# Kernel tuning notes

Hardware: AMD Instinct MI355X
Metric: run time of the kernel (lower is better)

The kernel has to match this reference:

```python
import jax, jax.numpy as jnp
import numpy as np

N, E, D, C, L = 50000, 800000, 128, 10, 3
TAU = 0.5
EPS = 1e-5


def _ln(h, g, b):
    m = jnp.mean(h, axis=-1, keepdims=True)
    v = jnp.mean((h - m) ** 2, axis=-1, keepdims=True)
    return (h - m) * jax.lax.rsqrt(v + EPS) * g + b


def _gumbel_hard(logits, gnoise, tau):
    # gumbel_softmax(hard=True): straight-through one-hot of softmax((logits+g)/tau)
    y_soft = jax.nn.softmax((logits + gnoise) / tau, axis=-1)
    idx = jnp.argmax(y_soft, axis=-1)
    y_hard = jax.nn.one_hot(idx, logits.shape[-1], dtype=y_soft.dtype)
    return jax.lax.stop_gradient(y_hard - y_soft) + y_soft


def setup_inputs() -> dict:
    key = jax.random.key(0)
    ks = jax.random.split(key, 20)
    s = lambda *sh: 1.0 / np.sqrt(sh[0])
    inp = {
        "x": jax.random.normal(ks[0], (N, D), jnp.float32),
        "edge_index": jax.random.randint(ks[1], (2, E), 0, N, jnp.int64),
        # encoder (node_encoder Linear in_dim->env_dim)
        "W_enc": jax.random.normal(ks[2], (D, D), jnp.float32) * s(D),
        "b_enc": jnp.zeros((D,), jnp.float32),
        # shared hidden LayerNorm
        "ln_g": jnp.ones((D,), jnp.float32),
        "ln_b": jnp.zeros((D,), jnp.float32),
        # env GNN layers (root / neighbor weights + bias), L layers
        "Wr": jax.random.normal(ks[3], (L, D, D), jnp.float32) * s(D),
        "Wn": jax.random.normal(ks[4], (L, D, D), jnp.float32) * s(D),
        "bl": jnp.zeros((L, D), jnp.float32),
        # in/out action nets (1 layer each, env_dim -> 2 logits)
        "Wa_in_r": jax.random.normal(ks[5], (D, 2), jnp.float32) * s(D),
        "Wa_in_n": jax.random.normal(ks[6], (D, 2), jnp.float32) * s(D),
        "ba_in": jnp.zeros((2,), jnp.float32),
        "Wa_out_r": jax.random.normal(ks[7], (D, 2), jnp.float32) * s(D),
        "Wa_out_n": jax.random.normal(ks[8], (D, 2), jnp.float32) * s(D),
        "ba_out": jnp.zeros((2,), jnp.float32),
        # decoder (dec_num_layers=1 -> single Linear env_dim -> num_classes)
        "W_dec": jax.random.normal(ks[9], (D, C), jnp.float32) * s(D),
        "b_dec": jnp.zeros((C,), jnp.float32),
        # pre-sampled Gumbel noise per layer for in/out action gates
        "gin": jax.random.gumbel(ks[10], (L, N, 2), jnp.float32),
        "gout": jax.random.gumbel(ks[11], (L, N, 2), jnp.float32),
    }
    return inp


def reference(x, edge_index, W_enc, b_enc, ln_g, ln_b, Wr, Wn, bl,
              Wa_in_r, Wa_in_n, ba_in, Wa_out_r, Wa_out_n, ba_out,
              W_dec, b_dec, gin, gout):
    u, v = edge_index[0], edge_index[1]
    n = x.shape[0]
    # node encoder + (use_encoders=False) dropout(0)+act
    h = jax.nn.relu(x @ W_enc + b_enc)
    node_states = []
    for l in range(L):
        hn = _ln(h, ln_g, ln_b)
        # unweighted neighbor aggregation shared by both action nets
        agg = jax.ops.segment_sum(hn[u], v, num_segments=n)  # [N, D]
        in_logits = hn @ Wa_in_r + agg @ Wa_in_n + ba_in
        out_logits = hn @ Wa_out_r + agg @ Wa_out_n + ba_out
        in_p = _gumbel_hard(in_logits, gin[l], TAU)
        out_p = _gumbel_hard(out_logits, gout[l], TAU)
        # edge gate: listen prob of target * broadcast prob of source
        ew = in_p[v, 0] * out_p[u, 0]  # [E]
        aggw = jax.ops.segment_sum(ew[:, None] * hn[u], v, num_segments=n)
        out = jax.nn.relu(hn @ Wr[l] + aggw @ Wn[l] + bl[l])
        # node state bookkeeping: 0 standard, 1 broadcast-only, 2 listen-only, 3 isolated
        act = jax.lax.stop_gradient(ew)
        is_b = (jax.ops.segment_max(act, u, num_segments=n) > 0.5).astype(jnp.int32)
        is_l = (jax.ops.segment_max(act, v, num_segments=n) > 0.5).astype(jnp.int32)
        node_states.append(3 - 2 * is_b - is_l)
        h = hn + out  # skip connection (onto the normalized x, as in the source)
    h = _ln(h, ln_g, ln_b)
    result = h @ W_dec + b_dec
    return result, jnp.stack(node_states)
```

## Files before the change

kernel.cpp:

```cpp
#include <hip/hip_runtime.h>

#define DIM 128
#define NCLS 10

__global__ void k_hist(const int* __restrict__ ei, int E, int* __restrict__ deg) {
    int e = blockIdx.x * 256 + threadIdx.x;
    if (e < E) atomicAdd(&deg[ei[E + e]], 1);
}

__global__ void k_scan1(const int* __restrict__ deg, int* __restrict__ row_start,
                        int* __restrict__ bsum, int n) {
    int tid = threadIdx.x;
    int base = blockIdx.x * 1024 + tid * 4;
    int v0 = 0, v1 = 0, v2 = 0, v3 = 0;
    if (base + 3 < n) {
        int4 t = *(const int4*)(deg + base);
        v0 = t.x; v1 = t.y; v2 = t.z; v3 = t.w;
    } else {
        if (base + 0 < n) v0 = deg[base + 0];
        if (base + 1 < n) v1 = deg[base + 1];
        if (base + 2 < n) v2 = deg[base + 2];
        if (base + 3 < n) v3 = deg[base + 3];
    }
    int s = v0 + v1 + v2 + v3;
    int lane = tid & 63, w = tid >> 6;
    int inc = s;
#pragma unroll
    for (int o = 1; o < 64; o <<= 1) {
        int t = __shfl_up(inc, o);
        if (lane >= o) inc += t;
    }
    __shared__ int wsum[4];
    if (lane == 63) wsum[w] = inc;
    __syncthreads();
    int woff = 0;
    for (int i = 0; i < w; i++) woff += wsum[i];
    int run = woff + inc - s;
    if (base + 0 < n) row_start[base + 0] = run; run += v0;
    if (base + 1 < n) row_start[base + 1] = run; run += v1;
    if (base + 2 < n) row_start[base + 2] = run; run += v2;
    if (base + 3 < n) row_start[base + 3] = run;
    if (tid == 0) bsum[blockIdx.x] = wsum[0] + wsum[1] + wsum[2] + wsum[3];
}

__global__ void k_scan2(int* __restrict__ bsum, int nb) {
    int tid = threadIdx.x;
    if (nb <= 64) {
        int v = (tid < nb) ? bsum[tid] : 0;
        int inc = v;
#pragma unroll
        for (int o = 1; o < 64; o <<= 1) {
            int t = __shfl_up(inc, o);
            if (tid >= o) inc += t;
        }
        if (tid < nb) bsum[tid] = inc - v;
    } else if (tid == 0) {
        int acc = 0;
        for (int i = 0; i < nb; i++) { int t = bsum[i]; bsum[i] = acc; acc += t; }
    }
}

__global__ void k_scan3(int* __restrict__ row_start, int* __restrict__ cursor,
                        const int* __restrict__ bsum, int n, int E) {
    int i = blockIdx.x * 256 + threadIdx.x;
    if (i < n) {
        int r = row_start[i] + bsum[i >> 10];
        row_start[i] = r;
        cursor[i] = r;
    }
    if (i == n) row_start[n] = E;
}

__global__ void k_fill(const int* __restrict__ ei, int E, int* __restrict__ cursor,
                       int* __restrict__ csr) {
    int e = blockIdx.x * 256 + threadIdx.x;
    if (e < E) {
        int u = ei[e], v = ei[E + e];
        int pos = atomicAdd(&cursor[v], 1);
        csr[pos] = u;
    }
}

__global__ void k_action(const float* __restrict__ proj, const int* __restrict__ row_start,
                         const int* __restrict__ csr,
                         const float* __restrict__ bain, const float* __restrict__ baon,
                         const float* __restrict__ gin_l, const float* __restrict__ gout_l,
                         int* __restrict__ in_bit, int* __restrict__ out_bit,
                         int* __restrict__ is_b, int n) {
    int v = blockIdx.x * 256 + threadIdx.x;
    if (v >= n) return;
    is_b[v] = 0;
    int b0 = row_start[v], b1 = row_start[v + 1];
    double a0 = 0.0, a1 = 0.0, a2 = 0.0, a3 = 0.0;
    for (int e = b0; e < b1; e++) {
        int u = csr[e];
        float4 p = *(const float4*)(proj + (size_t)u * 8);
        a0 += p.x; a1 += p.y; a2 += p.z; a3 += p.w;
    }
    float4 r = *(const float4*)(proj + (size_t)v * 8 + 4);
    float2 gi = *(const float2*)(gin_l + (size_t)v * 2);
    float2 go = *(const float2*)(gout_l + (size_t)v * 2);
    float li0 = (float)a0 + r.x + bain[0] + gi.x;
    float li1 = (float)a1 + r.y + bain[1] + gi.y;
    float lo0 = (float)a2 + r.z + baon[0] + go.x;
    float lo1 = (float)a3 + r.w + baon[1] + go.y;
    in_bit[v]  = (li0 >= li1) ? 1 : 0;
    out_bit[v] = (lo0 >= lo1) ? 1 : 0;
}

__global__ void k_aggw(const float* __restrict__ hn, const int* __restrict__ row_start,
                       const int* __restrict__ csr, const int* __restrict__ in_bit,
                       const int* __restrict__ out_bit,
                       int* __restrict__ is_b, int* __restrict__ is_l,
                       float* __restrict__ aggw, int n) {
    int wid = (blockIdx.x * 256 + threadIdx.x) >> 6;
    int lane = threadIdx.x & 63;
    if (wid >= n) return;
    int d0 = lane * 2;
    double ax = 0.0, ay = 0.0;
    int anyg = 0;
    if (in_bit[wid]) {
        int base = row_start[wid], end = row_start[wid + 1];
        for (int off = base; off < end; off += 64) {
            int m = min(64, end - off);
            int myu = 0, myb = 0;
            if (lane < m) { myu = csr[off + lane]; myb = out_bit[myu]; }
            unsigned long long mask = __ballot(myb != 0);
            anyg |= (mask != 0ull);
            while (mask) {
                int i = __ffsll((unsigned long long)mask) - 1;
                mask &= mask - 1;
                int u = __shfl(myu, i);
                if (lane == 0) is_b[u] = 1;
                float2 t = *(const float2*)(hn + (size_t)u * DIM + d0);
                ax += t.x; ay += t.y;
            }
        }
    }
    if (lane == 0) is_l[wid] = anyg;
    ((float2*)(aggw + (size_t)wid * DIM))[lane] = make_float2((float)ax, (float)ay);
}

template <int HAS_B, int SKIP, int DO_LN, int DO_PROJ, int DO_STATES, int DO_DEC, int WRITE_H>
__launch_bounds__(256)
__attribute__((amdgpu_waves_per_eu(4, 4)))
__global__ void k_gemm(const float* __restrict__ A, const float* __restrict__ W1,
                       const float* __restrict__ B, const float* __restrict__ W2,
                       const float* __restrict__ bias,
                       const float* __restrict__ ln_g, const float* __restrict__ ln_b,
                       const float* __restrict__ Wain, const float* __restrict__ Waon,
                       const float* __restrict__ Wair, const float* __restrict__ Waor,
                       const int* __restrict__ is_b, const int* __restrict__ is_l,
                       const float* __restrict__ Wdec, const float* __restrict__ bdec,
                       float* __restrict__ out, float* __restrict__ proj,
                       float* __restrict__ states_l, float* __restrict__ dec_out, int n) {
    __shared__ float sW[32][128];
    __shared__ float sA[64][36];
    int tid = threadIdx.x;
    int rowBase = blockIdx.x * 64;
    int ty = tid >> 4, tx = tid & 15;
    int c0 = tx * 4, c1 = 64 + tx * 4;
    float acc[4][8];
#pragma unroll
    for (int i = 0; i < 4; i++)
#pragma unroll
        for (int j = 0; j < 8; j++) acc[i][j] = 0.f;

    for (int p = 0; p < 1 + HAS_B; p++) {
        const float* Ap = p ? B : A;
        const float* Wp = p ? W2 : W1;
        for (int kc = 0; kc < DIM; kc += 32) {
            __syncthreads();
            {
                const float4* src = (const float4*)(Wp + kc * DIM);
                float4* dst = (float4*)(&sW[0][0]);
#pragma unroll
                for (int i = 0; i < 4; i++) {
                    int j = i * 256 + tid;
                    dst[j] = src[j];
                }
#pragma unroll
                for (int i = 0; i < 2; i++) {
                    int j = i * 256 + tid;
                    int r = j >> 3, c4 = (j & 7) * 4;
                    float4 va = (rowBase + r < n)
                        ? *(const float4*)(Ap + (size_t)(rowBase + r) * DIM + kc + c4)
                        : make_float4(0.f, 0.f, 0.f, 0.f);
                    *(float4*)&sA[r][c4] = va;
                }
            }
            __syncthreads();
#pragma unroll
            for (int kk = 0; kk < 32; kk += 4) {
                float4 a[4];
#pragma unroll
                for (int i = 0; i < 4; i++) a[i] = *(const float4*)&sA[i * 16 + ty][kk];
#pragma unroll
                for (int q = 0; q < 4; q++) {
                    float4 w0 = *(const float4*)&sW[kk + q][c0];
                    float4 w1 = *(const float4*)&sW[kk + q][c1];
#pragma unroll
                    for (int i = 0; i < 4; i++) {
                        float av = (&a[i].x)[q];
                        acc[i][0] += av * w0.x;
                        acc[i][1] += av * w0.y;
                        acc[i][2] += av * w0.z;
                        acc[i][3] += av * w0.w;
                        acc[i][4] += av * w1.x;
                        acc[i][5] += av * w1.y;
                        acc[i][6] += av * w1.z;
                        acc[i][7] += av * w1.w;
                    }
                }
            }
        }
    }

    float* sWd = (float*)&sW[0][0];
    if (DO_DEC) {
        __syncthreads();
        for (int i = tid; i < NCLS * DIM; i += 256) {
            int d = i / NCLS, c = i % NCLS;
            sWd[c * DIM + d] = Wdec[i];
        }
        __syncthreads();
    }

    float4 bias0 = *(const float4*)&bias[c0];
    float4 bias1 = *(const float4*)&bias[c1];
    float bv[8] = {bias0.x, bias0.y, bias0.z, bias0.w, bias1.x, bias1.y, bias1.z, bias1.w};
    float gv[8], bbv[8];
    if (DO_LN) {
        float4 g0 = *(const float4*)&ln_g[c0];
        float4 g1 = *(const float4*)&ln_g[c1];
        float4 lb0 = *(const float4*)&ln_b[c0];
        float4 lb1 = *(const float4*)&ln_b[c1];
        gv[0]=g0.x; gv[1]=g0.y; gv[2]=g0.z; gv[3]=g0.w; gv[4]=g1.x; gv[5]=g1.y; gv[6]=g1.z; gv[7]=g1.w;
        bbv[0]=lb0.x; bbv[1]=lb0.y; bbv[2]=lb0.z; bbv[3]=lb0.w; bbv[4]=lb1.x; bbv[5]=lb1.y; bbv[6]=lb1.z; bbv[7]=lb1.w;
    }

#pragma unroll
    for (int i = 0; i < 4; i++) {
        int r = rowBase + i * 16 + ty;
        if (r >= n) continue;
        float v[8];
        if (SKIP) {
            float4 s0 = *(const float4*)(A + (size_t)r * DIM + c0);
            float4 s1 = *(const float4*)(A + (size_t)r * DIM + c1);
            float sv[8] = {s0.x, s0.y, s0.z, s0.w, s1.x, s1.y, s1.z, s1.w};
#pragma unroll
            for (int j = 0; j < 8; j++) v[j] = fmaxf(acc[i][j] + bv[j], 0.f) + sv[j];
        } else {
#pragma unroll
            for (int j = 0; j < 8; j++) v[j] = fmaxf(acc[i][j] + bv[j], 0.f);
        }
        if (DO_LN) {
            float s = 0.f, q = 0.f;
#pragma unroll
            for (int j = 0; j < 8; j++) { s += v[j]; q += v[j] * v[j]; }
#pragma unroll
            for (int o = 1; o < 16; o <<= 1) { s += __shfl_xor(s, o); q += __shfl_xor(q, o); }
            float m = s * (1.f / DIM);
            float var = q * (1.f / DIM) - m * m;
            float inv = rsqrtf(var + 1e-5f);
#pragma unroll
            for (int j = 0; j < 8; j++) v[j] = (v[j] - m) * inv * gv[j] + bbv[j];
        }
        if (WRITE_H) {
            *(float4*)(out + (size_t)r * DIM + c0) = make_float4(v[0], v[1], v[2], v[3]);
            *(float4*)(out + (size_t)r * DIM + c1) = make_float4(v[4], v[5], v[6], v[7]);
        }
        if (DO_STATES) {
            if (tx == 0) states_l[r] = (float)(3 - 2 * is_b[r] - is_l[r]);
        }
        if (DO_PROJ) {
            float pv[8];
            auto dotw = [&](const float* Wm, float& p0, float& p1) {
                float4 q0 = *(const float4*)(Wm + c0 * 2);
                float4 q1 = *(const float4*)(Wm + c0 * 2 + 4);
                float4 q2 = *(const float4*)(Wm + c1 * 2);
                float4 q3 = *(const float4*)(Wm + c1 * 2 + 4);
                p0 = v[0]*q0.x + v[1]*q0.z + v[2]*q1.x + v[3]*q1.z
                   + v[4]*q2.x + v[5]*q2.z + v[6]*q3.x + v[7]*q3.z;
                p1 = v[0]*q0.y + v[1]*q0.w + v[2]*q1.y + v[3]*q1.w
                   + v[4]*q2.y + v[5]*q2.w + v[6]*q3.y + v[7]*q3.w;
            };
            dotw(Wain, pv[0], pv[1]);
            dotw(Waon, pv[2], pv[3]);
            dotw(Wair, pv[4], pv[5]);
            dotw(Waor, pv[6], pv[7]);
#pragma unroll
            for (int o = 1; o < 16; o <<= 1)
#pragma unroll
                for (int j = 0; j < 8; j++) pv[j] += __shfl_xor(pv[j], o);
            if (tx == 0) {
                *(float4*)(proj + (size_t)r * 8)     = make_float4(pv[0], pv[1], pv[2], pv[3]);
                *(float4*)(proj + (size_t)r * 8 + 4) = make_float4(pv[4], pv[5], pv[6], pv[7]);
            }
        }
        if (DO_DEC) {
            float p[NCLS];
#pragma unroll
            for (int c = 0; c < NCLS; c++) {
                float4 wd0 = *(const float4*)&sWd[c * DIM + c0];
                float4 wd1 = *(const float4*)&sWd[c * DIM + c1];
                p[c] = v[0]*wd0.x + v[1]*wd0.y + v[2]*wd0.z + v[3]*wd0.w
                     + v[4]*wd1.x + v[5]*wd1.y + v[6]*wd1.z + v[7]*wd1.w;
            }
#pragma unroll
            for (int o = 1; o < 16; o <<= 1)
#pragma unroll
                for (int c = 0; c < NCLS; c++) p[c] += __shfl_xor(p[c], o);
            if (tx == 0) {
#pragma unroll
                for (int c = 0; c < NCLS; c++) dec_out[(size_t)r * NCLS + c] = p[c] + bdec[c];
            }
        }
    }
}

extern "C" void kernel_launch(void* const* d_in, const int* in_sizes, int n_in,
                              void* d_out, int out_size, void* d_ws, size_t ws_size,
                              hipStream_t stream) {
    const float* x      = (const float*)d_in[0];
    const int*   ei     = (const int*)d_in[1];
    const float* W_enc  = (const float*)d_in[2];
    const float* b_enc  = (const float*)d_in[3];
    const float* ln_g   = (const float*)d_in[4];
    const float* ln_b   = (const float*)d_in[5];
    const float* Wr     = (const float*)d_in[6];
    const float* Wn     = (const float*)d_in[7];
    const float* bl     = (const float*)d_in[8];
    const float* Wair   = (const float*)d_in[9];
    const float* Wain   = (const float*)d_in[10];
    const float* bain   = (const float*)d_in[11];
    const float* Waor   = (const float*)d_in[12];
    const float* Waon   = (const float*)d_in[13];
    const float* baon   = (const float*)d_in[14];
    const float* W_dec  = (const float*)d_in[15];
    const float* b_dec  = (const float*)d_in[16];
    const float* gin    = (const float*)d_in[17];
    const float* gout   = (const float*)d_in[18];

    int n = in_sizes[0] / DIM;
    int E = in_sizes[1] / 2;
    const int L = 3;

    char* wsp = (char*)d_ws;
    auto alloc = [&](size_t bytes) { char* p = wsp; wsp += (bytes + 255) / 256 * 256; return p; };
    float* hn   = (float*)alloc((size_t)n * DIM * 4);
    float* aggw = (float*)alloc((size_t)n * DIM * 4);
    float* proj = (float*)alloc((size_t)n * 8 * 4);
    int* deg       = (int*)alloc((size_t)n * 4);
    int* row_start = (int*)alloc((size_t)(n + 1) * 4);
    int* cursor    = (int*)alloc((size_t)n * 4);
    int* csr       = (int*)alloc((size_t)E * 4);
    int* in_bit    = (int*)alloc((size_t)n * 4);
    int* out_bit   = (int*)alloc((size_t)n * 4);
    int* bsum      = (int*)alloc((size_t)256 * 4);
    int* is_b      = (int*)alloc((size_t)n * 4);
    int* is_l      = (int*)alloc((size_t)n * 4);

    float* out_res    = (float*)d_out;
    float* out_states = out_res + (size_t)n * NCLS;

    int ebl = (E + 255) / 256;
    int nbl = (n + 255) / 256;
    int wbl = (n + 3) / 4;
    int gbl = (n + 63) / 64;
    int nb  = (n + 1023) / 1024;

    hipMemsetAsync(deg, 0, (size_t)n * 4, stream);
    k_hist<<<ebl, 256, 0, stream>>>(ei, E, deg);
    k_scan1<<<nb, 256, 0, stream>>>(deg, row_start, bsum, n);
    k_scan2<<<1, 64, 0, stream>>>(bsum, nb);
    k_scan3<<<(n + 256) / 256, 256, 0, stream>>>(row_start, cursor, bsum, n, E);
    k_fill<<<ebl, 256, 0, stream>>>(ei, E, cursor, csr);

    k_gemm<0, 0, 1, 1, 0, 0, 1><<<gbl, 256, 0, stream>>>(
        x, W_enc, nullptr, nullptr, b_enc, ln_g, ln_b,
        Wain, Waon, Wair, Waor, nullptr, nullptr, nullptr, nullptr,
        hn, proj, nullptr, nullptr, n);

    for (int l = 0; l < L; l++) {
        k_action<<<nbl, 256, 0, stream>>>(proj, row_start, csr, bain, baon,
                                          gin + (size_t)l * n * 2, gout + (size_t)l * n * 2,
                                          in_bit, out_bit, is_b, n);
        k_aggw<<<wbl, 256, 0, stream>>>(hn, row_start, csr, in_bit, out_bit,
                                        is_b, is_l, aggw, n);
        if (l + 1 < L) {
            k_gemm<1, 1, 1, 1, 1, 0, 1><<<gbl, 256, 0, stream>>>(
                hn, Wr + (size_t)l * DIM * DIM, aggw, Wn + (size_t)l * DIM * DIM,
                bl + (size_t)l * DIM, ln_g, ln_b,
                Wain, Waon, Wair, Waor, is_b, is_l, nullptr, nullptr,
                hn, proj, out_states + (size_t)l * n, nullptr, n);
        } else {
            k_gemm<1, 1, 1, 0, 1, 1, 0><<<gbl, 256, 0, stream>>>(
                hn, Wr + (size_t)l * DIM * DIM, aggw, Wn + (size_t)l * DIM * DIM,
                bl + (size_t)l * DIM, ln_g, ln_b,
                Wain, Waon, Wair, Waor, is_b, is_l, W_dec, b_dec,
                hn, nullptr, out_states + (size_t)l * n, out_res, n);
        }
    }
}
```

Measured before the change: 485.3 us.

## Project node features before aggregation to run GEMMs ahead of gated gather

Uses linearity to compute hn·Wr and hn·Wn in one two-column-block GEMM before the gated neighbour sum. A new post kernel then gathers the projected rows, adds bias, ReLU, the skip connection and LayerNorm, and computes the action projections or decoder logits. This removes the dependence of the GEMM on the aggregated tensor and fuses the epilogue into the gather pass. In exchange it writes and reads two N×D intermediates per layer instead of one, and the gather now sums projected values in a different order. State output is moved into k_action plus a final small kernel.

```diff
diff --git a/kernel.cpp b/kernel.cpp
--- a/kernel.cpp
+++ b/kernel.cpp
@@ -86,9 +86,11 @@
                          const float* __restrict__ bain, const float* __restrict__ baon,
                          const float* __restrict__ gin_l, const float* __restrict__ gout_l,
                          int* __restrict__ in_bit, int* __restrict__ out_bit,
-                         int* __restrict__ is_b, int n) {
+                         int* __restrict__ is_b, const int* __restrict__ is_l,
+                         float* __restrict__ states_prev, int n) {
     int v = blockIdx.x * 256 + threadIdx.x;
     if (v >= n) return;
+    if (states_prev) states_prev[v] = (float)(3 - 2 * is_b[v] - is_l[v]);
     is_b[v] = 0;
     int b0 = row_start[v], b1 = row_start[v + 1];
     double a0 = 0.0, a1 = 0.0, a2 = 0.0, a3 = 0.0;
@@ -108,15 +110,170 @@
     out_bit[v] = (lo0 >= lo1) ? 1 : 0;
 }
 
-__global__ void k_aggw(const float* __restrict__ hn, const int* __restrict__ row_start,
-                       const int* __restrict__ csr, const int* __restrict__ in_bit,
-                       const int* __restrict__ out_bit,
+template <int ENC>
+__launch_bounds__(256)
+__attribute__((amdgpu_waves_per_eu(4, 4)))
+__global__ void k_gemm(const float* __restrict__ A,
+                       const float* __restrict__ W1, const float* __restrict__ W2,
+                       const float* __restrict__ bias,
+                       const float* __restrict__ ln_g, const float* __restrict__ ln_b,
+                       const float* __restrict__ Wain, const float* __restrict__ Waon,
+                       const float* __restrict__ Wair, const float* __restrict__ Waor,
+                       float* __restrict__ out1, float* __restrict__ out2,
+                       float* __restrict__ proj, int n) {
+    __shared__ float sW[32][128];
+    __shared__ float sA[64][36];
+    int tid = threadIdx.x;
+    int rowBase = blockIdx.y * 64;
+    const float* Wp = (ENC || blockIdx.x == 0) ? W1 : W2;
+    float* outp = (ENC || blockIdx.x == 0) ? out1 : out2;
+    int ty = tid >> 4, tx = tid & 15;
+    int c0 = tx * 4, c1 = 64 + tx * 4;
+    float acc[4][8];
+#pragma unroll
+    for (int i = 0; i < 4; i++)
+#pragma unroll
+        for (int j = 0; j < 8; j++) acc[i][j] = 0.f;
+
+    for (int kc = 0; kc < DIM; kc += 32) {
+        __syncthreads();
+        {
+            const float4* src = (const float4*)(Wp + kc * DIM);
+            float4* dst = (float4*)(&sW[0][0]);
+#pragma unroll
+            for (int i = 0; i < 4; i++) {
+                int j = i * 256 + tid;
+                dst[j] = src[j];
+            }
+#pragma unroll
+            for (int i = 0; i < 2; i++) {
+                int j = i * 256 + tid;
+                int r = j >> 3, c4 = (j & 7) * 4;
+                float4 va = (rowBase + r < n)
+                    ? *(const float4*)(A + (size_t)(rowBase + r) * DIM + kc + c4)
+                    : make_float4(0.f, 0.f, 0.f, 0.f);
+                *(float4*)&sA[r][c4] = va;
+            }
+        }
+        __syncthreads();
+#pragma unroll
+        for (int kk = 0; kk < 32; kk += 4) {
+            float4 a[4];
+#pragma unroll
+            for (int i = 0; i < 4; i++) a[i] = *(const float4*)&sA[i * 16 + ty][kk];
+#pragma unroll
+            for (int q = 0; q < 4; q++) {
+                float4 w0 = *(const float4*)&sW[kk + q][c0];
+                float4 w1 = *(const float4*)&sW[kk + q][c1];
+#pragma unroll
+                for (int i = 0; i < 4; i++) {
+                    float av = (&a[i].x)[q];
+                    acc[i][0] += av * w0.x;
+                    acc[i][1] += av * w0.y;
+                    acc[i][2] += av * w0.z;
+                    acc[i][3] += av * w0.w;
+                    acc[i][4] += av * w1.x;
+                    acc[i][5] += av * w1.y;
+                    acc[i][6] += av * w1.z;
+                    acc[i][7] += av * w1.w;
+                }
+            }
+        }
+    }
+
+    if (!ENC) {
+#pragma unroll
+        for (int i = 0; i < 4; i++) {
+            int r = rowBase + i * 16 + ty;
+            if (r >= n) continue;
+            *(float4*)(outp + (size_t)r * DIM + c0) = make_float4(acc[i][0], acc[i][1], acc[i][2], acc[i][3]);
+            *(float4*)(outp + (size_t)r * DIM + c1) = make_float4(acc[i][4], acc[i][5], acc[i][6], acc[i][7]);
+        }
+        return;
+    }
+
+    float4 bias0 = *(const float4*)&bias[c0];
+    float4 bias1 = *(const float4*)&bias[c1];
+    float bv[8] = {bias0.x, bias0.y, bias0.z, bias0.w, bias1.x, bias1.y, bias1.z, bias1.w};
+    float4 g0 = *(const float4*)&ln_g[c0];
+    float4 g1 = *(const float4*)&ln_g[c1];
+    float4 lb0 = *(const float4*)&ln_b[c0];
+    float4 lb1 = *(const float4*)&ln_b[c1];
+    float gv[8]  = {g0.x, g0.y, g0.z, g0.w, g1.x, g1.y, g1.z, g1.w};
+    float bbv[8] = {lb0.x, lb0.y, lb0.z, lb0.w, lb1.x, lb1.y, lb1.z, lb1.w};
+
+#pragma unroll
+    for (int i = 0; i < 4; i++) {
+        int r = rowBase + i * 16 + ty;
+        if (r >= n) continue;
+        float v[8];
+#pragma unroll
+        for (int j = 0; j < 8; j++) v[j] = fmaxf(acc[i][j] + bv[j], 0.f);
+        float s = 0.f, q = 0.f;
+#pragma unroll
+        for (int j = 0; j < 8; j++) { s += v[j]; q += v[j] * v[j]; }
+#pragma unroll
+        for (int o = 1; o < 16; o <<= 1) { s += __shfl_xor(s, o); q += __shfl_xor(q, o); }
+        float m = s * (1.f / DIM);
+        float var = q * (1.f / DIM) - m * m;
+        float inv = rsqrtf(var + 1e-5f);
+#pragma unroll
+        for (int j = 0; j < 8; j++) v[j] = (v[j] - m) * inv * gv[j] + bbv[j];
+        *(float4*)(out1 + (size_t)r * DIM + c0) = make_float4(v[0], v[1], v[2], v[3]);
+        *(float4*)(out1 + (size_t)r * DIM + c1) = make_float4(v[4], v[5], v[6], v[7]);
+
+        float pv[8];
+        auto dotw = [&](const float* Wm, float& p0, float& p1) {
+            float4 q0 = *(const float4*)(Wm + c0 * 2);
+            float4 q1 = *(const float4*)(Wm + c0 * 2 + 4);
+            float4 q2 = *(const float4*)(Wm + c1 * 2);
+            float4 q3 = *(const float4*)(Wm + c1 * 2 + 4);
+            p0 = v[0]*q0.x + v[1]*q0.z + v[2]*q1.x + v[3]*q1.z
+               + v[4]*q2.x + v[5]*q2.z + v[6]*q3.x + v[7]*q3.z;
+            p1 = v[0]*q0.y + v[1]*q0.w + v[2]*q1.y + v[3]*q1.w
+               + v[4]*q2.y + v[5]*q2.w + v[6]*q3.y + v[7]*q3.w;
+        };
+        dotw(Wain, pv[0], pv[1]);
+        dotw(Waon, pv[2], pv[3]);
+        dotw(Wair, pv[4], pv[5]);
+        dotw(Waor, pv[6], pv[7]);
+#pragma unroll
+        for (int o = 1; o < 16; o <<= 1)
+#pragma unroll
+            for (int j = 0; j < 8; j++) pv[j] += __shfl_xor(pv[j], o);
+        if (tx == 0) {
+            *(float4*)(proj + (size_t)r * 8)     = make_float4(pv[0], pv[1], pv[2], pv[3]);
+            *(float4*)(proj + (size_t)r * 8 + 4) = make_float4(pv[4], pv[5], pv[6], pv[7]);
+        }
+    }
+}
+
+template <int DO_PROJ, int DO_DEC>
+__global__ void k_post(const float* __restrict__ y, const float* __restrict__ z,
+                       float* __restrict__ hn,
+                       const int* __restrict__ row_start, const int* __restrict__ csr,
+                       const int* __restrict__ in_bit, const int* __restrict__ out_bit,
                        int* __restrict__ is_b, int* __restrict__ is_l,
-                       float* __restrict__ aggw, int n) {
-    int wid = (blockIdx.x * 256 + threadIdx.x) >> 6;
-    int lane = threadIdx.x & 63;
+                       const float* __restrict__ bl_l,
+                       const float* __restrict__ ln_g, const float* __restrict__ ln_b,
+                       const float* __restrict__ Wain, const float* __restrict__ Waon,
+                       const float* __restrict__ Wair, const float* __restrict__ Waor,
+                       const float* __restrict__ Wdec, const float* __restrict__ bdec,
+                       float* __restrict__ proj, float* __restrict__ dec_out, int n) {
+    __shared__ float sWd[NCLS * DIM];
+    int tid = threadIdx.x;
+    if (DO_DEC) {
+        for (int i = tid; i < NCLS * DIM; i += 256) {
+            int d = i / NCLS, c = i % NCLS;
+            sWd[c * DIM + d] = Wdec[i];
+        }
+        __syncthreads();
+    }
+    int wid = (blockIdx.x * 256 + tid) >> 6;
+    int lane = tid & 63;
     if (wid >= n) return;
     int d0 = lane * 2;
+
     double ax = 0.0, ay = 0.0;
     int anyg = 0;
     if (in_bit[wid]) {
@@ -132,191 +289,74 @@
                 mask &= mask - 1;
                 int u = __shfl(myu, i);
                 if (lane == 0) is_b[u] = 1;
-                float2 t = *(const float2*)(hn + (size_t)u * DIM + d0);
+                float2 t = *(const float2*)(z + (size_t)u * DIM + d0);
                 ax += t.x; ay += t.y;
             }
         }
     }
     if (lane == 0) is_l[wid] = anyg;
-    ((float2*)(aggw + (size_t)wid * DIM))[lane] = make_float2((float)ax, (float)ay);
-}
-
-template <int HAS_B, int SKIP, int DO_LN, int DO_PROJ, int DO_STATES, int DO_DEC, int WRITE_H>
-__launch_bounds__(256)
-__attribute__((amdgpu_waves_per_eu(4, 4)))
-__global__ void k_gemm(const float* __restrict__ A, const float* __restrict__ W1,
-                       const float* __restrict__ B, const float* __restrict__ W2,
-                       const float* __restrict__ bias,
-                       const float* __restrict__ ln_g, const float* __restrict__ ln_b,
-                       const float* __restrict__ Wain, const float* __restrict__ Waon,
-                       const float* __restrict__ Wair, const float* __restrict__ Waor,
-                       const int* __restrict__ is_b, const int* __restrict__ is_l,
-                       const float* __restrict__ Wdec, const float* __restrict__ bdec,
-                       float* __restrict__ out, float* __restrict__ proj,
-                       float* __restrict__ states_l, float* __restrict__ dec_out, int n) {
-    __shared__ float sW[32][128];
-    __shared__ float sA[64][36];
-    int tid = threadIdx.x;
-    int rowBase = blockIdx.x * 64;
-    int ty = tid >> 4, tx = tid & 15;
-    int c0 = tx * 4, c1 = 64 + tx * 4;
-    float acc[4][8];
-#pragma unroll
-    for (int i = 0; i < 4; i++)
-#pragma unroll
-        for (int j = 0; j < 8; j++) acc[i][j] = 0.f;
-
-    for (int p = 0; p < 1 + HAS_B; p++) {
-        const float* Ap = p ? B : A;
-        const float* Wp = p ? W2 : W1;
-        for (int kc = 0; kc < DIM; kc += 32) {
-            __syncthreads();
-            {
-                const float4* src = (const float4*)(Wp + kc * DIM);
-                float4* dst = (float4*)(&sW[0][0]);
-#pragma unroll
-                for (int i = 0; i < 4; i++) {
-                    int j = i * 256 + tid;
-                    dst[j] = src[j];
-                }
-#pragma unroll
-                for (int i = 0; i < 2; i++) {
-                    int j = i * 256 + tid;
-                    int r = j >> 3, c4 = (j & 7) * 4;
-                    float4 va = (rowBase + r < n)
-                        ? *(const float4*)(Ap + (size_t)(rowBase + r) * DIM + kc + c4)
-                        : make_float4(0.f, 0.f, 0.f, 0.f);
-                    *(float4*)&sA[r][c4] = va;
-                }
-            }
-            __syncthreads();
-#pragma unroll
-            for (int kk = 0; kk < 32; kk += 4) {
-                float4 a[4];
-#pragma unroll
-                for (int i = 0; i < 4; i++) a[i] = *(const float4*)&sA[i * 16 + ty][kk];
-#pragma unroll
-                for (int q = 0; q < 4; q++) {
-                    float4 w0 = *(const float4*)&sW[kk + q][c0];
-                    float4 w1 = *(const float4*)&sW[kk + q][c1];
-#pragma unroll
-                    for (int i = 0; i < 4; i++) {
-                        float av = (&a[i].x)[q];
-                        acc[i][0] += av * w0.x;
-                        acc[i][1] += av * w0.y;
-                        acc[i][2] += av * w0.z;
-                        acc[i][3] += av * w0.w;
-                        acc[i][4] += av * w1.x;
-                        acc[i][5] += av * w1.y;
-                        acc[i][6] += av * w1.z;
-                        acc[i][7] += av * w1.w;
-                    }
-                }
-            }
-        }
-    }
-
-    float* sWd = (float*)&sW[0][0];
+
+    float2 yv = *(const float2*)(y + (size_t)wid * DIM + d0);
+    float2 h2 = *(const float2*)(hn + (size_t)wid * DIM + d0);
+    float2 b2 = *(const float2*)(bl_l + d0);
+    float vx = h2.x + fmaxf(yv.x + (float)ax + b2.x, 0.f);
+    float vy = h2.y + fmaxf(yv.y + (float)ay + b2.y, 0.f);
+
+    float s = vx + vy, q = vx * vx + vy * vy;
+#pragma unroll
+    for (int o = 32; o; o >>= 1) { s += __shfl_xor(s, o); q += __shfl_xor(q, o); }
+    float m = s * (1.f / DIM);
+    float var = q * (1.f / DIM) - m * m;
+    float inv = rsqrtf(var + 1e-5f);
+    float2 g2 = *(const float2*)(ln_g + d0);
+    float2 lb2 = *(const float2*)(ln_b + d0);
+    float ox = (vx - m) * inv * g2.x + lb2.x;
+    float oy = (vy - m) * inv * g2.y + lb2.y;
+
+    if (!DO_DEC)
+        *(float2*)(hn + (size_t)wid * DIM + d0) = make_float2(ox, oy);
+
+    if (DO_PROJ) {
+        float4 win = *(const float4*)(Wain + d0 * 2);
+        float4 won = *(const float4*)(Waon + d0 * 2);
+        float4 wir = *(const float4*)(Wair + d0 * 2);
+        float4 wor = *(const float4*)(Waor + d0 * 2);
+        float p[8];
+        p[0] = ox * win.x + oy * win.z;  p[1] = ox * win.y + oy * win.w;
+        p[2] = ox * won.x + oy * won.z;  p[3] = ox * won.y + oy * won.w;
+        p[4] = ox * wir.x + oy * wir.z;  p[5] = ox * wir.y + oy * wir.w;
+        p[6] = ox * wor.x + oy * wor.z;  p[7] = ox * wor.y + oy * wor.w;
+#pragma unroll
+        for (int o = 32; o; o >>= 1)
+#pragma unroll
+            for (int j = 0; j < 8; j++) p[j] += __shfl_xor(p[j], o);
+        if (lane == 0) {
+            *(float4*)(proj + (size_t)wid * 8)     = make_float4(p[0], p[1], p[2], p[3]);
+            *(float4*)(proj + (size_t)wid * 8 + 4) = make_float4(p[4], p[5], p[6], p[7]);
+        }
+    }
     if (DO_DEC) {
-        __syncthreads();
-        for (int i = tid; i < NCLS * DIM; i += 256) {
-            int d = i / NCLS, c = i % NCLS;
-            sWd[c * DIM + d] = Wdec[i];
-        }
-        __syncthreads();
-    }
-
-    float4 bias0 = *(const float4*)&bias[c0];
-    float4 bias1 = *(const float4*)&bias[c1];
-    float bv[8] = {bias0.x, bias0.y, bias0.z, bias0.w, bias1.x, bias1.y, bias1.z, bias1.w};
-    float gv[8], bbv[8];
-    if (DO_LN) {
-        float4 g0 = *(const float4*)&ln_g[c0];
-        float4 g1 = *(const float4*)&ln_g[c1];
-        float4 lb0 = *(const float4*)&ln_b[c0];
-        float4 lb1 = *(const float4*)&ln_b[c1];
-        gv[0]=g0.x; gv[1]=g0.y; gv[2]=g0.z; gv[3]=g0.w; gv[4]=g1.x; gv[5]=g1.y; gv[6]=g1.z; gv[7]=g1.w;
-        bbv[0]=lb0.x; bbv[1]=lb0.y; bbv[2]=lb0.z; bbv[3]=lb0.w; bbv[4]=lb1.x; bbv[5]=lb1.y; bbv[6]=lb1.z; bbv[7]=lb1.w;
-    }
-
-#pragma unroll
-    for (int i = 0; i < 4; i++) {
-        int r = rowBase + i * 16 + ty;
-        if (r >= n) continue;
-        float v[8];
-        if (SKIP) {
-            float4 s0 = *(const float4*)(A + (size_t)r * DIM + c0);
-            float4 s1 = *(const float4*)(A + (size_t)r * DIM + c1);
-            float sv[8] = {s0.x, s0.y, s0.z, s0.w, s1.x, s1.y, s1.z, s1.w};
-#pragma unroll
-            for (int j = 0; j < 8; j++) v[j] = fmaxf(acc[i][j] + bv[j], 0.f) + sv[j];
-        } else {
-#pragma unroll
-            for (int j = 0; j < 8; j++) v[j] = fmaxf(acc[i][j] + bv[j], 0.f);
-        }
-        if (DO_LN) {
-            float s = 0.f, q = 0.f;
-#pragma unroll
-            for (int j = 0; j < 8; j++) { s += v[j]; q += v[j] * v[j]; }
-#pragma unroll
-            for (int o = 1; o < 16; o <<= 1) { s += __shfl_xor(s, o); q += __shfl_xor(q, o); }
-            float m = s * (1.f / DIM);
-            float var = q * (1.f / DIM) - m * m;
-            float inv = rsqrtf(var + 1e-5f);
-#pragma unroll
-            for (int j = 0; j < 8; j++) v[j] = (v[j] - m) * inv * gv[j] + bbv[j];
-        }
-        if (WRITE_H) {
-            *(float4*)(out + (size_t)r * DIM + c0) = make_float4(v[0], v[1], v[2], v[3]);
-            *(float4*)(out + (size_t)r * DIM + c1) = make_float4(v[4], v[5], v[6], v[7]);
-        }
-        if (DO_STATES) {
-            if (tx == 0) states_l[r] = (float)(3 - 2 * is_b[r] - is_l[r]);
-        }
-        if (DO_PROJ) {
-            float pv[8];
-            auto dotw = [&](const float* Wm, float& p0, float& p1) {
-                float4 q0 = *(const float4*)(Wm + c0 * 2);
-                float4 q1 = *(const float4*)(Wm + c0 * 2 + 4);
-                float4 q2 = *(const float4*)(Wm + c1 * 2);
-                float4 q3 = *(const float4*)(Wm + c1 * 2 + 4);
-                p0 = v[0]*q0.x + v[1]*q0.z + v[2]*q1.x + v[3]*q1.z
-                   + v[4]*q2.x + v[5]*q2.z + v[6]*q3.x + v[7]*q3.z;
-                p1 = v[0]*q0.y + v[1]*q0.w + v[2]*q1.y + v[3]*q1.w
-                   + v[4]*q2.y + v[5]*q2.w + v[6]*q3.y + v[7]*q3.w;
-            };
-            dotw(Wain, pv[0], pv[1]);
-            dotw(Waon, pv[2], pv[3]);
-            dotw(Wair, pv[4], pv[5]);
-            dotw(Waor, pv[6], pv[7]);
-#pragma unroll
-            for (int o = 1; o < 16; o <<= 1)
-#pragma unroll
-                for (int j = 0; j < 8; j++) pv[j] += __shfl_xor(pv[j], o);
-            if (tx == 0) {
-                *(float4*)(proj + (size_t)r * 8)     = make_float4(pv[0], pv[1], pv[2], pv[3]);
-                *(float4*)(proj + (size_t)r * 8 + 4) = make_float4(pv[4], pv[5], pv[6], pv[7]);
-            }
-        }
-        if (DO_DEC) {
-            float p[NCLS];
-#pragma unroll
-            for (int c = 0; c < NCLS; c++) {
-                float4 wd0 = *(const float4*)&sWd[c * DIM + c0];
-                float4 wd1 = *(const float4*)&sWd[c * DIM + c1];
-                p[c] = v[0]*wd0.x + v[1]*wd0.y + v[2]*wd0.z + v[3]*wd0.w
-                     + v[4]*wd1.x + v[5]*wd1.y + v[6]*wd1.z + v[7]*wd1.w;
-            }
-#pragma unroll
-            for (int o = 1; o < 16; o <<= 1)
-#pragma unroll
-                for (int c = 0; c < NCLS; c++) p[c] += __shfl_xor(p[c], o);
-            if (tx == 0) {
-#pragma unroll
-                for (int c = 0; c < NCLS; c++) dec_out[(size_t)r * NCLS + c] = p[c] + bdec[c];
-            }
-        }
-    }
+        float p[NCLS];
+#pragma unroll
+        for (int c = 0; c < NCLS; c++) {
+            float2 w = *(const float2*)(&sWd[c * DIM + d0]);
+            p[c] = ox * w.x + oy * w.y;
+        }
+#pragma unroll
+        for (int o = 32; o; o >>= 1)
+#pragma unroll
+            for (int c = 0; c < NCLS; c++) p[c] += __shfl_xor(p[c], o);
+        if (lane == 0) {
+#pragma unroll
+            for (int c = 0; c < NCLS; c++) dec_out[(size_t)wid * NCLS + c] = p[c] + bdec[c];
+        }
+    }
+}
+
+__global__ void k_states(const int* __restrict__ is_b, const int* __restrict__ is_l,
+                         float* __restrict__ st, int n) {
+    int i = blockIdx.x * 256 + threadIdx.x;
+    if (i < n) st[i] = (float)(3 - 2 * is_b[i] - is_l[i]);
 }
 
 extern "C" void kernel_launch(void* const* d_in, const int* in_sizes, int n_in,
@@ -349,7 +389,8 @@
     char* wsp = (char*)d_ws;
     auto alloc = [&](size_t bytes) { char* p = wsp; wsp += (bytes + 255) / 256 * 256; return p; };
     float* hn   = (float*)alloc((size_t)n * DIM * 4);
-    float* aggw = (float*)alloc((size_t)n * DIM * 4);
+    float* yb   = (float*)alloc((size_t)n * DIM * 4);
+    float* zb   = (float*)alloc((size_t)n * DIM * 4);
     float* proj = (float*)alloc((size_t)n * 8 * 4);
     int* deg       = (int*)alloc((size_t)n * 4);
     int* row_start = (int*)alloc((size_t)(n + 1) * 4);
@@ -377,29 +418,33 @@
     k_scan3<<<(n + 256) / 256, 256, 0, stream>>>(row_start, cursor, bsum, n, E);
     k_fill<<<ebl, 256, 0, stream>>>(ei, E, cursor, csr);
 
-    k_gemm<0, 0, 1, 1, 0, 0, 1><<<gbl, 256, 0, stream>>>(
-        x, W_enc, nullptr, nullptr, b_enc, ln_g, ln_b,
-        Wain, Waon, Wair, Waor, nullptr, nullptr, nullptr, nullptr,
-        hn, proj, nullptr, nullptr, n);
+    k_gemm<1><<<dim3(1, gbl), 256, 0, stream>>>(
+        x, W_enc, nullptr, b_enc, ln_g, ln_b,
+        Wain, Waon, Wair, Waor, hn, nullptr, proj, n);
 
     for (int l = 0; l < L; l++) {
-        k_action<<<nbl, 256, 0, stream>>>(proj, row_start, csr, bain, baon,
-                                          gin + (size_t)l * n * 2, gout + (size_t)l * n * 2,
-                                          in_bit, out_bit, is_b, n);
-        k_aggw<<<wbl, 256, 0, stream>>>(hn, row_start, csr, in_bit, out_bit,
-                                        is_b, is_l, aggw, n);
+        k_action<<<nbl, 256, 0, stream>>>(
+            proj, row_start, csr, bain, baon,
+            gin + (size_t)l * n * 2, gout + (size_t)l * n * 2,
+            in_bit, out_bit, is_b, is_l,
+            l ? out_states + (size_t)(l - 1) * n : nullptr, n);
+        k_gemm<0><<<dim3(2, gbl), 256, 0, stream>>>(
+            hn, Wr + (size_t)l * DIM * DIM, Wn + (size_t)l * DIM * DIM,
+            nullptr, nullptr, nullptr,
+            nullptr, nullptr, nullptr, nullptr, yb, zb, nullptr, n);
         if (l + 1 < L) {
-            k_gemm<1, 1, 1, 1, 1, 0, 1><<<gbl, 256, 0, stream>>>(
-                hn, Wr + (size_t)l * DIM * DIM, aggw, Wn + (size_t)l * DIM * DIM,
+            k_post<1, 0><<<wbl, 256, 0, stream>>>(
+                yb, zb, hn, row_start, csr, in_bit, out_bit, is_b, is_l,
                 bl + (size_t)l * DIM, ln_g, ln_b,
-                Wain, Waon, Wair, Waor, is_b, is_l, nullptr, nullptr,
-                hn, proj, out_states + (size_t)l * n, nullptr, n);
+                Wain, Waon, Wair, Waor, nullptr, nullptr,
+                proj, nullptr, n);
         } else {
-            k_gemm<1, 1, 1, 0, 1, 1, 0><<<gbl, 256, 0, stream>>>(
-                hn, Wr + (size_t)l * DIM * DIM, aggw, Wn + (size_t)l * DIM * DIM,
+            k_post<0, 1><<<wbl, 256, 0, stream>>>(
+                yb, zb, hn, row_start, csr, in_bit, out_bit, is_b, is_l,
                 bl + (size_t)l * DIM, ln_g, ln_b,
-                Wain, Waon, Wair, Waor, is_b, is_l, W_dec, b_dec,
-                hn, nullptr, out_states + (size_t)l * n, out_res, n);
-        }
-    }
-}
+                Wain, Waon, Wair, Waor, W_dec, b_dec,
+                nullptr, out_res, n);
+        }
+    }
+    k_states<<<nbl, 256, 0, stream>>>(is_b, is_l, out_states + (size_t)(L - 1) * n, n);
+}
```

Measured after the change: 527.1 us. 8.6% more time.

## Double-buffer GEMM shared-memory tiles with register prefetch of next k-chunk

Applied to the files above, without the earlier changes.

The GEMM mainloop now keeps two shared-memory buffers for the weight and activation tiles. The next k-chunk is loaded into registers while the current one is computed, then committed to the other buffer, so there is one barrier per chunk instead of two. This aims to hide global-load latency behind the FMA work. It doubles LDS use and adds prefetch registers, so the occupancy hint is relaxed to 2-4 waves per EU, which may lower occupancy.

```diff
diff --git a/kernel.cpp b/kernel.cpp
--- a/kernel.cpp
+++ b/kernel.cpp
@@ -143,7 +143,7 @@
 
 template <int HAS_B, int SKIP, int DO_LN, int DO_PROJ, int DO_STATES, int DO_DEC, int WRITE_H>
 __launch_bounds__(256)
-__attribute__((amdgpu_waves_per_eu(4, 4)))
+__attribute__((amdgpu_waves_per_eu(2, 4)))
 __global__ void k_gemm(const float* __restrict__ A, const float* __restrict__ W1,
                        const float* __restrict__ B, const float* __restrict__ W2,
                        const float* __restrict__ bias,
@@ -154,71 +154,79 @@
                        const float* __restrict__ Wdec, const float* __restrict__ bdec,
                        float* __restrict__ out, float* __restrict__ proj,
                        float* __restrict__ states_l, float* __restrict__ dec_out, int n) {
-    __shared__ float sW[32][128];
-    __shared__ float sA[64][36];
+    __shared__ float sW[2][32][128];
+    __shared__ float sA[2][64][36];
     int tid = threadIdx.x;
     int rowBase = blockIdx.x * 64;
     int ty = tid >> 4, tx = tid & 15;
     int c0 = tx * 4, c1 = 64 + tx * 4;
+    const int T = 4 * (1 + HAS_B);
+    int lr = tid >> 3, lc4 = (tid & 7) * 4;
+
     float acc[4][8];
 #pragma unroll
     for (int i = 0; i < 4; i++)
 #pragma unroll
         for (int j = 0; j < 8; j++) acc[i][j] = 0.f;
 
-    for (int p = 0; p < 1 + HAS_B; p++) {
-        const float* Ap = p ? B : A;
-        const float* Wp = p ? W2 : W1;
-        for (int kc = 0; kc < DIM; kc += 32) {
-            __syncthreads();
-            {
-                const float4* src = (const float4*)(Wp + kc * DIM);
-                float4* dst = (float4*)(&sW[0][0]);
+    float4 wpre[4], apre0, apre1;
+    auto prefetch = [&](int t) {
+        const float* Ap = (HAS_B && t >= 4) ? B : A;
+        const float* Wp = (HAS_B && t >= 4) ? W2 : W1;
+        int kc = (t & 3) * 32;
+        const float4* src = (const float4*)(Wp + kc * DIM);
+#pragma unroll
+        for (int i = 0; i < 4; i++) wpre[i] = src[tid + i * 256];
+        apre0 = (rowBase + lr < n)
+            ? *(const float4*)(Ap + (size_t)(rowBase + lr) * DIM + kc + lc4)
+            : make_float4(0.f, 0.f, 0.f, 0.f);
+        apre1 = (rowBase + lr + 32 < n)
+            ? *(const float4*)(Ap + (size_t)(rowBase + lr + 32) * DIM + kc + lc4)
+            : make_float4(0.f, 0.f, 0.f, 0.f);
+    };
+    auto commit = [&](int b) {
+        float4* dst = (float4*)(&sW[b][0][0]);
+#pragma unroll
+        for (int i = 0; i < 4; i++) dst[tid + i * 256] = wpre[i];
+        *(float4*)&sA[b][lr][lc4] = apre0;
+        *(float4*)&sA[b][lr + 32][lc4] = apre1;
+    };
+
+    prefetch(0);
+    commit(0);
+    __syncthreads();
+    for (int t = 0; t < T; t++) {
+        int b = t & 1;
+        if (t + 1 < T) prefetch(t + 1);
+#pragma unroll
+        for (int kk = 0; kk < 32; kk += 4) {
+            float4 a[4];
+#pragma unroll
+            for (int i = 0; i < 4; i++) a[i] = *(const float4*)&sA[b][i * 16 + ty][kk];
+#pragma unroll
+            for (int q = 0; q < 4; q++) {
+                float4 w0 = *(const float4*)&sW[b][kk + q][c0];
+                float4 w1 = *(const float4*)&sW[b][kk + q][c1];
 #pragma unroll
                 for (int i = 0; i < 4; i++) {
-                    int j = i * 256 + tid;
-                    dst[j] = src[j];
-                }
-#pragma unroll
-                for (int i = 0; i < 2; i++) {
-                    int j = i * 256 + tid;
-                    int r = j >> 3, c4 = (j & 7) * 4;
-                    float4 va = (rowBase + r < n)
-                        ? *(const float4*)(Ap + (size_t)(rowBase + r) * DIM + kc + c4)
-                        : make_float4(0.f, 0.f, 0.f, 0.f);
-                    *(float4*)&sA[r][c4] = va;
+                    float av = (&a[i].x)[q];
+                    acc[i][0] += av * w0.x;
+                    acc[i][1] += av * w0.y;
+                    acc[i][2] += av * w0.z;
+                    acc[i][3] += av * w0.w;
+                    acc[i][4] += av * w1.x;
+                    acc[i][5] += av * w1.y;
+                    acc[i][6] += av * w1.z;
+                    acc[i][7] += av * w1.w;
                 }
             }
-            __syncthreads();
-#pragma unroll
-            for (int kk = 0; kk < 32; kk += 4) {
-                float4 a[4];
-#pragma unroll
-                for (int i = 0; i < 4; i++) a[i] = *(const float4*)&sA[i * 16 + ty][kk];
-#pragma unroll
-                for (int q = 0; q < 4; q++) {
-                    float4 w0 = *(const float4*)&sW[kk + q][c0];
-                    float4 w1 = *(const float4*)&sW[kk + q][c1];
-#pragma unroll
-                    for (int i = 0; i < 4; i++) {
-                        float av = (&a[i].x)[q];
-                        acc[i][0] += av * w0.x;
-                        acc[i][1] += av * w0.y;
-                        acc[i][2] += av * w0.z;
-                        acc[i][3] += av * w0.w;
-                        acc[i][4] += av * w1.x;
-                        acc[i][5] += av * w1.y;
-                        acc[i][6] += av * w1.z;
-                        acc[i][7] += av * w1.w;
-                    }
-                }
-            }
-        }
-    }
-
-    float* sWd = (float*)&sW[0][0];
+        }
+        if (t + 1 < T) commit(b ^ 1);
+        __syncthreads();
+    }
+
+    float* sWd = (float*)&sW[0][0][0];
     if (DO_DEC) {
-        __syncthreads();
         for (int i = tid; i < NCLS * DIM; i += 256) {
             int d = i / NCLS, c = i % NCLS;
             sWd[c * DIM + d] = Wdec[i];
```

Result: slower. 1.930 ms (+297.6%).
